# Kernel tuning notes

Hardware: AMD Instinct MI355X
Metric: run time of the kernel (lower is better)

Reference implementation:

```python
import jax, jax.numpy as jnp
import numpy as np

H = 8  # num_heads

def setup_inputs() -> dict:
    key = jax.random.key(0)
    ks = jax.random.split(key, 10)
    B, N, C = 2048, 50, 256
    x = jax.random.normal(ks[0], (B, N, C), dtype=jnp.float32)
    adj = jax.random.uniform(ks[1], (B, N, N), dtype=jnp.float32)
    matrix = jax.random.normal(ks[2], (B, N, N), dtype=jnp.float32)
    s = 0.02
    Wq = jax.random.normal(ks[3], (C, C), dtype=jnp.float32) * s
    bq = jnp.zeros((C,), dtype=jnp.float32)
    Wk = jax.random.normal(ks[4], (C, C), dtype=jnp.float32) * s
    bk = jnp.zeros((C,), dtype=jnp.float32)
    Wa = jax.random.normal(ks[5], (N * H, N), dtype=jnp.float32) * s
    ba = jnp.zeros((N * H,), dtype=jnp.float32)
    Wm = jax.random.normal(ks[6], (N * H, N), dtype=jnp.float32) * s
    bm = jnp.zeros((N * H,), dtype=jnp.float32)
    lambdas = jnp.tile(jnp.array([[1.0, 0.0, 0.0]], dtype=jnp.float32), (H, 1))
    return {"x": x, "adj": adj, "matrix": matrix, "Wq": Wq, "bq": bq,
            "Wk": Wk, "bk": bk, "Wa": Wa, "ba": ba, "Wm": Wm, "bm": bm,
            "lambdas": lambdas}

def reference(x, adj, matrix, Wq, bq, Wk, bk, Wa, ba, Wm, bm, lambdas):
    B, N, C = x.shape
    D = C // H
    # torch Linear: y = x @ W.T + b
    q = (jnp.einsum('bnc,dc->bnd', x, Wq) + bq).reshape(B, N, H, D).transpose(0, 2, 1, 3)
    k = (jnp.einsum('bnc,dc->bnd', x, Wk) + bk).reshape(B, N, H, D).transpose(0, 2, 1, 3)
    # NOTE: original code computes v with self.k (faithful to source)
    v = k
    # scale uses full dim C (x.shape[-1]), not head_dim, as in source
    attn = jax.nn.softmax(jnp.einsum('bhnd,bhmd->bhnm', q, k) * (C ** -0.5), axis=-1)
    adj_a = jax.nn.softmax(
        (jnp.einsum('bnm,km->bnk', adj, Wa) + ba).reshape(B, N, H, N).transpose(0, 2, 1, 3), axis=-1)
    mat_a = jax.nn.softmax(
        (jnp.einsum('bnm,km->bnk', matrix, Wm) + bm).reshape(B, N, H, N).transpose(0, 2, 1, 3), axis=-1)
    lam = jax.nn.softmax(lambdas, axis=-1)  # [H, 3]
    l0 = lam[:, 0][None, :, None, None]
    l1 = lam[:, 1][None, :, None, None]
    l2 = lam[:, 2][None, :, None, None]
    mix = l0 * attn + l1 * adj_a + l2 * mat_a  # [B, H, N, N]
    out = jnp.einsum('bhnm,bhmd->bhnd', mix, v).transpose(0, 2, 1, 3).reshape(B, N, C)
    return out
```

## Files before the change

kernel.cpp:

```cpp
#include <hip/hip_runtime.h>
#include <stdint.h>


typedef __attribute__((ext_vector_type(8))) short short8;
typedef __attribute__((ext_vector_type(4))) float f32x4;
typedef unsigned short u16;

__device__ __forceinline__ u16 f2bf(float f) {
  unsigned int u = __float_as_uint(f);
  u = (u + 0x7FFFu + ((u >> 16) & 1u)) >> 16;
  return (u16)u;
}
__device__ __forceinline__ unsigned cvt_pk_bf16(float a, float b) {
  unsigned r;
  asm("v_cvt_pk_bf16_f32 %0, %1, %2" : "=v"(r) : "v"(a), "v"(b));
  return r;
}

__global__ __launch_bounds__(256) void castW(const float* __restrict__ Wq,
                                             const float* __restrict__ Wk,
                                             u16* __restrict__ dst) {
  int idx8 = blockIdx.x * 256 + threadIdx.x;
  int r = idx8 >> 5, c = (idx8 & 31) * 8;
  const float* src = (r < 256) ? (Wq + (size_t)r * 256 + c)
                               : (Wk + (size_t)(r - 256) * 256 + c);
  float4 v0 = *(const float4*)(src);
  float4 v1 = *(const float4*)(src + 4);
  short8 o;
  o[0] = f2bf(v0.x); o[1] = f2bf(v0.y); o[2] = f2bf(v0.z); o[3] = f2bf(v0.w);
  o[4] = f2bf(v1.x); o[5] = f2bf(v1.y); o[6] = f2bf(v1.z); o[7] = f2bf(v1.w);
  *(short8*)(dst + (size_t)idx8 * 8) = o;
}

__global__ __launch_bounds__(256) void castS(const float* __restrict__ Wa,
                                             const float* __restrict__ Wm,
                                             u16* __restrict__ da, u16* __restrict__ dm) {
  int idx = blockIdx.x * 256 + threadIdx.x;
  int r = idx >> 6, c = idx & 63;
  float va = 0.f, vm = 0.f;
  if (r < 400 && c < 50) { va = Wa[r * 50 + c]; vm = Wm[r * 50 + c]; }
  da[idx] = f2bf(va); dm[idx] = f2bf(vm);
}

__global__ __launch_bounds__(256) void castA(const float* __restrict__ adj,
                                             const float* __restrict__ mat,
                                             u16* __restrict__ da, u16* __restrict__ dm) {
  const int total8 = (102416 * 64) / 8;
  int stride = gridDim.x * 256;
  for (int i8 = blockIdx.x * 256 + threadIdx.x; i8 < total8; i8 += stride) {
    int r = i8 >> 3, c = (i8 & 7) * 8;
    short8 oa = (short8){0,0,0,0,0,0,0,0};
    short8 om = (short8){0,0,0,0,0,0,0,0};
    if (r < 102400) {
      size_t base = (size_t)r * 50;
#pragma unroll
      for (int p = 0; p < 4; ++p) {
        int col = c + 2 * p;
        if (col < 50) {
          float2 va = *(const float2*)(adj + base + col);
          float2 vm = *(const float2*)(mat + base + col);
          oa[2*p] = f2bf(va.x); oa[2*p+1] = f2bf(va.y);
          om[2*p] = f2bf(vm.x); om[2*p+1] = f2bf(vm.y);
        }
      }
    }
    *(short8*)(da + (size_t)i8 * 8) = oa;
    *(short8*)(dm + (size_t)i8 * 8) = om;
  }
}

__global__ __launch_bounds__(256) void proj_kernel(
    const float* __restrict__ x, const u16* __restrict__ wqk,
    const float* __restrict__ bq, const float* __restrict__ bk,
    u16* __restrict__ qws, u16* __restrict__ kws) {
  __shared__ char xa[64 * 512];
  __shared__ char wb[64 * 512];
  const int tid = threadIdx.x;
  const int m0 = blockIdx.x * 64;

#pragma unroll
  for (int t = 0; t < 16; ++t) {
    int idx = tid + t * 256;
    int r = idx >> 6, c4 = idx & 63;
    float4 v = *(const float4*)(x + (size_t)(m0 + r) * 256 + c4 * 4);
    unsigned long long pk = (unsigned long long)f2bf(v.x)
                          | ((unsigned long long)f2bf(v.y) << 16)
                          | ((unsigned long long)f2bf(v.z) << 32)
                          | ((unsigned long long)f2bf(v.w) << 48);
    int byte = (r * 512 + c4 * 8) ^ ((r & 7) << 4);
    *(unsigned long long*)(xa + byte) = pk;
  }
  __syncthreads();

  const int w = tid >> 6, l = tid & 63, lo = l & 15, g = l >> 4;
  short8 a[8];
  const int ra = 16 * w + lo;
#pragma unroll
  for (int ks = 0; ks < 8; ++ks)
    a[ks] = *(const short8*)(xa + ((ra * 512 + ks * 64 + g * 16) ^ ((ra & 7) << 4)));
  size_t mb[4];
#pragma unroll
  for (int i = 0; i < 4; ++i) {
    int m = m0 + 16 * w + 4 * g + i;
    int b = m / 50;
    int n = m - 50 * b;
    mb[i] = (size_t)b * 12800 + (size_t)n * 32;
  }

  for (int nt = 0; nt < 8; ++nt) {
    __syncthreads();
#pragma unroll
    for (int t = 0; t < 8; ++t) {
      int idx = tid + t * 256;
      int r = idx >> 5, c8 = idx & 31;
      short8 v = *(const short8*)(wqk + (size_t)(nt * 64 + r) * 256 + c8 * 8);
      int byte = (r * 512 + c8 * 16) ^ ((r & 7) << 4);
      *(short8*)(wb + byte) = v;
    }
    __syncthreads();

    f32x4 acc[4];
#pragma unroll
    for (int tj = 0; tj < 4; ++tj) acc[tj] = (f32x4){0.f, 0.f, 0.f, 0.f};
#pragma unroll
    for (int ks = 0; ks < 8; ++ks) {
#pragma unroll
      for (int tj = 0; tj < 4; ++tj) {
        int rb = 16 * tj + lo;
        short8 bb = *(const short8*)(wb + ((rb * 512 + ks * 64 + g * 16) ^ ((rb & 7) << 4)));
        acc[tj] = __builtin_amdgcn_mfma_f32_16x16x32_bf16(a[ks], bb, acc[tj], 0, 0, 0);
      }
    }
    const int n0 = nt * 64;
#pragma unroll
    for (int tj = 0; tj < 4; ++tj) {
      int j = n0 + 16 * tj + lo;
      int jj = j & 255;
      float bias = (j < 256) ? bq[jj] : bk[jj];
      u16* dst = (j < 256) ? qws : kws;
      int hh = jj >> 5, d = jj & 31;
#pragma unroll
      for (int i = 0; i < 4; ++i)
        dst[mb[i] + (size_t)hh * 1600 + d] = f2bf(acc[tj][i] + bias);
    }
  }
}


__device__ __forceinline__ void lds_fence() {
  asm volatile("s_waitcnt lgkmcnt(0)" ::: "memory");
  __builtin_amdgcn_sched_barrier(0);
}

__device__ __forceinline__ void softmax_store(f32x4 (&S)[4], const float (&bias)[4][4],
                                              float scale, float lam,
                                              u16* sh, int tj, int lo, int g) {
  float mx = -3.0e38f;
#pragma unroll
  for (int ti = 0; ti < 4; ++ti)
#pragma unroll
    for (int i = 0; i < 4; ++i) {
      float v = S[ti][i] * scale + bias[ti][i];
      S[ti][i] = v;
      mx = fmaxf(mx, v);
    }
  mx = fmaxf(mx, __shfl_xor(mx, 16));
  mx = fmaxf(mx, __shfl_xor(mx, 32));
  float sum = 0.f;
#pragma unroll
  for (int ti = 0; ti < 4; ++ti)
#pragma unroll
    for (int i = 0; i < 4; ++i) {
      float p = __expf(S[ti][i] - mx);
      S[ti][i] = p;
      sum += p;
    }
  sum += __shfl_xor(sum, 16);
  sum += __shfl_xor(sum, 32);
  float r = lam * __builtin_amdgcn_rcpf(sum);
  const int n = lo + 16 * tj;
#pragma unroll
  for (int ti = 0; ti < 4; ++ti) {
    uint2 pk;
    pk.x = cvt_pk_bf16(S[ti][0] * r, S[ti][1] * r);
    pk.y = cvt_pk_bf16(S[ti][2] * r, S[ti][3] * r);
    *(uint2*)(sh + n * 72 + 16 * ti + 4 * g) = pk;
  }
}

__device__ __forceinline__ void pv_accum(const u16* sh, const short8 (&vb)[2][2],
                                         f32x4 (&O)[4][2], int lo, int g) {
  lds_fence();
#pragma unroll
  for (int ks = 0; ks < 2; ++ks) {
    short8 pa[4];
#pragma unroll
    for (int ti = 0; ti < 4; ++ti)
      pa[ti] = *(const short8*)(sh + (lo + 16 * ti) * 72 + ks * 32 + g * 8);
#pragma unroll
    for (int tjv = 0; tjv < 2; ++tjv)
#pragma unroll
      for (int ti = 0; ti < 4; ++ti)
        O[ti][tjv] = __builtin_amdgcn_mfma_f32_16x16x32_bf16(pa[ti], vb[tjv][ks], O[ti][tjv], 0, 0, 0);
  }
}

__device__ __forceinline__ void adj_phase(const u16* __restrict__ aBase,
                                          const u16* __restrict__ bBase,
                                          const float* __restrict__ biasPtr,
                                          float lam, u16* sh, const short8 (&vb)[2][2],
                                          f32x4 (&O)[4][2], int lo, int g) {
  short8 af[4][2];
#pragma unroll
  for (int ti = 0; ti < 4; ++ti)
#pragma unroll
    for (int ks = 0; ks < 2; ++ks)
      af[ti][ks] = *(const short8*)(aBase + (size_t)(lo + 16 * ti) * 64 + ks * 32 + g * 8);
  float bias[4][4];
#pragma unroll
  for (int ti = 0; ti < 4; ++ti)
#pragma unroll
    for (int i = 0; i < 4; ++i) {
      int m = 16 * ti + 4 * g + i;
      bias[ti][i] = (m < 50) ? biasPtr[m] : -1.0e30f;
    }
#pragma unroll
  for (int tj = 0; tj < 4; ++tj) {
    f32x4 S[4];
#pragma unroll
    for (int ti = 0; ti < 4; ++ti) S[ti] = (f32x4){0.f, 0.f, 0.f, 0.f};
#pragma unroll
    for (int ks = 0; ks < 2; ++ks) {
      short8 bf8 = *(const short8*)(bBase + (size_t)(lo + 16 * tj) * 64 + ks * 32 + g * 8);
#pragma unroll
      for (int ti = 0; ti < 4; ++ti)
        S[ti] = __builtin_amdgcn_mfma_f32_16x16x32_bf16(af[ti][ks], bf8, S[ti], 0, 0, 0);
    }
    softmax_store(S, bias, 1.0f, lam, sh, tj, lo, g);
  }
  pv_accum(sh, vb, O, lo, g);
}

__global__ __launch_bounds__(256) void attn_kernel(
    const u16* __restrict__ qws, const u16* __restrict__ kws,
    const u16* __restrict__ adjb, const u16* __restrict__ matb,
    const u16* __restrict__ wab, const u16* __restrict__ wmb,
    const float* __restrict__ ba, const float* __restrict__ bm,
    const float* __restrict__ lambdas, float* __restrict__ out) {
  __shared__ u16 smem[4][4608];
  const int tid = threadIdx.x;
  const int w = tid >> 6, l = tid & 63, lo = l & 15, g = l >> 4;
  const int bh = blockIdx.x * 4 + w;
  const int b = bh >> 3, h = bh & 7;
  u16* sh = smem[w];

  float la = lambdas[h * 3 + 0], lb = lambdas[h * 3 + 1], lc = lambdas[h * 3 + 2];
  float lmx = fmaxf(la, fmaxf(lb, lc));
  float e0 = __expf(la - lmx), e1 = __expf(lb - lmx), e2 = __expf(lc - lmx);
  float einv = 1.f / (e0 + e1 + e2);
  float lam0 = e0 * einv, lam1 = e1 * einv, lam2 = e2 * einv;

  {
    const u16* kr = kws + ((size_t)bh * 50 + l) * 32;
#pragma unroll
    for (int ch = 0; ch < 4; ++ch) {
      short8 v = (short8){0, 0, 0, 0, 0, 0, 0, 0};
      if (l < 50) v = *(const short8*)(kr + ch * 8);
#pragma unroll
      for (int jj = 0; jj < 8; ++jj)
        sh[(ch * 8 + jj) * 72 + l] = (u16)v[jj];
    }
  }
  lds_fence();
  short8 vb[2][2];
#pragma unroll
  for (int tjv = 0; tjv < 2; ++tjv)
#pragma unroll
    for (int ks = 0; ks < 2; ++ks)
      vb[tjv][ks] = *(const short8*)(sh + (lo + 16 * tjv) * 72 + ks * 32 + g * 8);

  f32x4 O[4][2];
#pragma unroll
  for (int ti = 0; ti < 4; ++ti)
#pragma unroll
    for (int tjv = 0; tjv < 2; ++tjv) O[ti][tjv] = (f32x4){0.f, 0.f, 0.f, 0.f};

  {
    short8 af[4];
#pragma unroll
    for (int ti = 0; ti < 4; ++ti)
      af[ti] = *(const short8*)(kws + ((size_t)bh * 50 + lo + 16 * ti) * 32 + g * 8);
    float bias[4][4];
#pragma unroll
    for (int ti = 0; ti < 4; ++ti)
#pragma unroll
      for (int i = 0; i < 4; ++i)
        bias[ti][i] = (16 * ti + 4 * g + i < 50) ? 0.f : -1.0e30f;
#pragma unroll
    for (int tj = 0; tj < 4; ++tj) {
      short8 qf = *(const short8*)(qws + ((size_t)bh * 50 + lo + 16 * tj) * 32 + g * 8);
      f32x4 S[4];
#pragma unroll
      for (int ti = 0; ti < 4; ++ti) S[ti] = (f32x4){0.f, 0.f, 0.f, 0.f};
#pragma unroll
      for (int ti = 0; ti < 4; ++ti)
        S[ti] = __builtin_amdgcn_mfma_f32_16x16x32_bf16(af[ti], qf, S[ti], 0, 0, 0);
      softmax_store(S, bias, 0.0625f, lam0, sh, tj, lo, g);
    }
    pv_accum(sh, vb, O, lo, g);
  }
  adj_phase(wab + (size_t)h * 50 * 64, adjb + (size_t)b * 50 * 64, ba + h * 50,
            lam1, sh, vb, O, lo, g);
  adj_phase(wmb + (size_t)h * 50 * 64, matb + (size_t)b * 50 * 64, bm + h * 50,
            lam2, sh, vb, O, lo, g);

  float* ob = out + ((size_t)b * 50) * 256 + h * 32;
#pragma unroll
  for (int ti = 0; ti < 4; ++ti)
#pragma unroll
    for (int i = 0; i < 4; ++i) {
      int n = 16 * ti + 4 * g + i;
      if (n < 50) {
#pragma unroll
        for (int tjv = 0; tjv < 2; ++tjv)
          ob[(size_t)n * 256 + 16 * tjv + lo] = O[ti][tjv][i];
      }
    }
}

extern "C" void kernel_launch(void* const* d_in, const int* in_sizes, int n_in,
                              void* d_out, int out_size, void* d_ws, size_t ws_size,
                              hipStream_t stream) {
  const float* x       = (const float*)d_in[0];
  const float* adj     = (const float*)d_in[1];
  const float* mat     = (const float*)d_in[2];
  const float* Wq      = (const float*)d_in[3];
  const float* bq      = (const float*)d_in[4];
  const float* Wk      = (const float*)d_in[5];
  const float* bk      = (const float*)d_in[6];
  const float* Wa      = (const float*)d_in[7];
  const float* ba      = (const float*)d_in[8];
  const float* Wm      = (const float*)d_in[9];
  const float* bm      = (const float*)d_in[10];
  const float* lambdas = (const float*)d_in[11];
  float* out = (float*)d_out;

  char* ws = (char*)d_ws;
  u16* wqk  = (u16*)ws; ws += (size_t)512 * 256 * 2;
  u16* wab  = (u16*)ws; ws += (size_t)416 * 64 * 2;
  u16* wmb  = (u16*)ws; ws += (size_t)416 * 64 * 2;
  u16* adjb = (u16*)ws; ws += (size_t)102416 * 64 * 2;
  u16* matb = (u16*)ws; ws += (size_t)102416 * 64 * 2;
  u16* qws  = (u16*)ws; ws += (size_t)819264 * 32 * 2;
  u16* kws  = (u16*)ws; ws += (size_t)819264 * 32 * 2;

  castW<<<64, 256, 0, stream>>>(Wq, Wk, wqk);
  castS<<<104, 256, 0, stream>>>(Wa, Wm, wab, wmb);
  castA<<<2048, 256, 0, stream>>>(adj, mat, adjb, matb);
  proj_kernel<<<1600, 256, 0, stream>>>(x, wqk, bq, bk, qws, kws);
  attn_kernel<<<4096, 256, 0, stream>>>(qws, kws, adjb, matb, wab, wmb, ba, bm, lambdas, out);
}
```

Before: 218.9 us.

## Merge cast kernels and fuse per-tile softmax with PV accumulation

Folds the three cast launches into one kernel that also zeroes the padding rows of the q/k workspace. The attention softmax is restructured to process one query tile at a time and immediately feed it into the PV MFMAs through a double-buffered LDS slot. This halves shared memory per block and shortens register live ranges. The max-subtraction is dropped and exp2 is used with log2e folded into scale and bias. Skipping the max is only safe while logits stay small, which adds overflow risk for larger inputs.

```diff
diff --git a/kernel.cpp b/kernel.cpp
--- a/kernel.cpp
+++ b/kernel.cpp
@@ -5,6 +5,8 @@
 typedef __attribute__((ext_vector_type(8))) short short8;
 typedef __attribute__((ext_vector_type(4))) float f32x4;
 typedef unsigned short u16;
+
+#define L2E 1.4426950408889634f
 
 __device__ __forceinline__ u16 f2bf(float f) {
   unsigned int u = __float_as_uint(f);
@@ -16,56 +18,68 @@
   asm("v_cvt_pk_bf16_f32 %0, %1, %2" : "=v"(r) : "v"(a), "v"(b));
   return r;
 }
-
-__global__ __launch_bounds__(256) void castW(const float* __restrict__ Wq,
-                                             const float* __restrict__ Wk,
-                                             u16* __restrict__ dst) {
-  int idx8 = blockIdx.x * 256 + threadIdx.x;
-  int r = idx8 >> 5, c = (idx8 & 31) * 8;
-  const float* src = (r < 256) ? (Wq + (size_t)r * 256 + c)
-                               : (Wk + (size_t)(r - 256) * 256 + c);
-  float4 v0 = *(const float4*)(src);
-  float4 v1 = *(const float4*)(src + 4);
-  short8 o;
-  o[0] = f2bf(v0.x); o[1] = f2bf(v0.y); o[2] = f2bf(v0.z); o[3] = f2bf(v0.w);
-  o[4] = f2bf(v1.x); o[5] = f2bf(v1.y); o[6] = f2bf(v1.z); o[7] = f2bf(v1.w);
-  *(short8*)(dst + (size_t)idx8 * 8) = o;
-}
-
-__global__ __launch_bounds__(256) void castS(const float* __restrict__ Wa,
-                                             const float* __restrict__ Wm,
-                                             u16* __restrict__ da, u16* __restrict__ dm) {
-  int idx = blockIdx.x * 256 + threadIdx.x;
-  int r = idx >> 6, c = idx & 63;
-  float va = 0.f, vm = 0.f;
-  if (r < 400 && c < 50) { va = Wa[r * 50 + c]; vm = Wm[r * 50 + c]; }
-  da[idx] = f2bf(va); dm[idx] = f2bf(vm);
-}
-
-__global__ __launch_bounds__(256) void castA(const float* __restrict__ adj,
-                                             const float* __restrict__ mat,
-                                             u16* __restrict__ da, u16* __restrict__ dm) {
-  const int total8 = (102416 * 64) / 8;
-  int stride = gridDim.x * 256;
-  for (int i8 = blockIdx.x * 256 + threadIdx.x; i8 < total8; i8 += stride) {
-    int r = i8 >> 3, c = (i8 & 7) * 8;
-    short8 oa = (short8){0,0,0,0,0,0,0,0};
-    short8 om = (short8){0,0,0,0,0,0,0,0};
-    if (r < 102400) {
-      size_t base = (size_t)r * 50;
-#pragma unroll
-      for (int p = 0; p < 4; ++p) {
-        int col = c + 2 * p;
-        if (col < 50) {
-          float2 va = *(const float2*)(adj + base + col);
-          float2 vm = *(const float2*)(mat + base + col);
-          oa[2*p] = f2bf(va.x); oa[2*p+1] = f2bf(va.y);
-          om[2*p] = f2bf(vm.x); om[2*p+1] = f2bf(vm.y);
+__device__ __forceinline__ float exp2_fast(float x) {
+#if __has_builtin(__builtin_amdgcn_exp2f)
+  return __builtin_amdgcn_exp2f(x);
+#else
+  return __expf(x * 0.6931471805599453f);
+#endif
+}
+__device__ __forceinline__ void lds_fence() {
+  asm volatile("s_waitcnt lgkmcnt(0)" ::: "memory");
+}
+
+__global__ __launch_bounds__(256) void cast_all(
+    const float* __restrict__ adj, const float* __restrict__ mat,
+    const float* __restrict__ Wq, const float* __restrict__ Wk,
+    const float* __restrict__ Wa, const float* __restrict__ Wm,
+    u16* __restrict__ da, u16* __restrict__ dm, u16* __restrict__ wqk,
+    u16* __restrict__ wab, u16* __restrict__ wmb,
+    u16* __restrict__ qws, u16* __restrict__ kws) {
+  const int blk = blockIdx.x, tid = threadIdx.x;
+  if (blk < 2048) {
+    const int total8 = (102416 * 64) / 8;
+    for (int i8 = blk * 256 + tid; i8 < total8; i8 += 2048 * 256) {
+      int r = i8 >> 3, c = (i8 & 7) * 8;
+      short8 oa = (short8){0,0,0,0,0,0,0,0};
+      short8 om = (short8){0,0,0,0,0,0,0,0};
+      if (r < 102400) {
+        size_t base = (size_t)r * 50;
+#pragma unroll
+        for (int p = 0; p < 4; ++p) {
+          int col = c + 2 * p;
+          if (col < 50) {
+            float2 va = *(const float2*)(adj + base + col);
+            float2 vm = *(const float2*)(mat + base + col);
+            oa[2*p] = f2bf(va.x); oa[2*p+1] = f2bf(va.y);
+            om[2*p] = f2bf(vm.x); om[2*p+1] = f2bf(vm.y);
+          }
         }
       }
-    }
-    *(short8*)(da + (size_t)i8 * 8) = oa;
-    *(short8*)(dm + (size_t)i8 * 8) = om;
+      *(short8*)(da + (size_t)i8 * 8) = oa;
+      *(short8*)(dm + (size_t)i8 * 8) = om;
+    }
+  } else if (blk < 2112) {
+    int idx8 = (blk - 2048) * 256 + tid;
+    int r = idx8 >> 5, c = (idx8 & 31) * 8;
+    const float* src = (r < 256) ? (Wq + (size_t)r * 256 + c)
+                                 : (Wk + (size_t)(r - 256) * 256 + c);
+    float4 v0 = *(const float4*)(src);
+    float4 v1 = *(const float4*)(src + 4);
+    short8 o;
+    o[0] = f2bf(v0.x); o[1] = f2bf(v0.y); o[2] = f2bf(v0.z); o[3] = f2bf(v0.w);
+    o[4] = f2bf(v1.x); o[5] = f2bf(v1.y); o[6] = f2bf(v1.z); o[7] = f2bf(v1.w);
+    *(short8*)(wqk + (size_t)idx8 * 8) = o;
+  } else if (blk < 2216) {
+    int idx = (blk - 2112) * 256 + tid;
+    int r = idx >> 6, c = idx & 63;
+    float va = 0.f, vm = 0.f;
+    if (r < 400 && c < 50) { va = Wa[r * 50 + c]; vm = Wm[r * 50 + c]; }
+    wab[idx] = f2bf(va); wmb[idx] = f2bf(vm);
+  } else {
+    short8 z = (short8){0,0,0,0,0,0,0,0};
+    *(short8*)(qws + (size_t)819200 * 32 + tid * 8) = z;
+    *(short8*)(kws + (size_t)819200 * 32 + tid * 8) = z;
   }
 }
 
@@ -146,99 +160,74 @@
   }
 }
 
-
-__device__ __forceinline__ void lds_fence() {
-  asm volatile("s_waitcnt lgkmcnt(0)" ::: "memory");
-  __builtin_amdgcn_sched_barrier(0);
-}
-
-__device__ __forceinline__ void softmax_store(f32x4 (&S)[4], const float (&bias)[4][4],
-                                              float scale, float lam,
-                                              u16* sh, int tj, int lo, int g) {
-  float mx = -3.0e38f;
-#pragma unroll
-  for (int ti = 0; ti < 4; ++ti)
-#pragma unroll
-    for (int i = 0; i < 4; ++i) {
-      float v = S[ti][i] * scale + bias[ti][i];
-      S[ti][i] = v;
-      mx = fmaxf(mx, v);
-    }
-  mx = fmaxf(mx, __shfl_xor(mx, 16));
-  mx = fmaxf(mx, __shfl_xor(mx, 32));
-  float sum = 0.f;
-#pragma unroll
-  for (int ti = 0; ti < 4; ++ti)
-#pragma unroll
-    for (int i = 0; i < 4; ++i) {
-      float p = __expf(S[ti][i] - mx);
-      S[ti][i] = p;
-      sum += p;
-    }
+__device__ __forceinline__ void sm_pv_tile(
+    f32x4 (&S)[4], const float (&bml)[4][4], float sl2e, float lam,
+    u16* pb, const short8 (&vb)[2][2], f32x4 (&Otj)[2], int tj, int lo, int g) {
+  float p[4][4];
+#pragma unroll
+  for (int ti = 0; ti < 4; ++ti)
+#pragma unroll
+    for (int i = 0; i < 4; ++i)
+      p[ti][i] = exp2_fast(S[ti][i] * sl2e + bml[ti][i]);
+  float t0 = (p[0][0] + p[0][1]) + (p[0][2] + p[0][3]);
+  float t1 = (p[1][0] + p[1][1]) + (p[1][2] + p[1][3]);
+  float t2 = (p[2][0] + p[2][1]) + (p[2][2] + p[2][3]);
+  float t3 = (p[3][0] + p[3][1]) + (p[3][2] + p[3][3]);
+  float sum = (t0 + t1) + (t2 + t3);
   sum += __shfl_xor(sum, 16);
   sum += __shfl_xor(sum, 32);
   float r = lam * __builtin_amdgcn_rcpf(sum);
-  const int n = lo + 16 * tj;
+  u16* base = pb + (tj & 1) * 1152 + lo * 72;
 #pragma unroll
   for (int ti = 0; ti < 4; ++ti) {
     uint2 pk;
-    pk.x = cvt_pk_bf16(S[ti][0] * r, S[ti][1] * r);
-    pk.y = cvt_pk_bf16(S[ti][2] * r, S[ti][3] * r);
-    *(uint2*)(sh + n * 72 + 16 * ti + 4 * g) = pk;
-  }
-}
-
-__device__ __forceinline__ void pv_accum(const u16* sh, const short8 (&vb)[2][2],
-                                         f32x4 (&O)[4][2], int lo, int g) {
+    pk.x = cvt_pk_bf16(p[ti][0] * r, p[ti][1] * r);
+    pk.y = cvt_pk_bf16(p[ti][2] * r, p[ti][3] * r);
+    *(uint2*)(base + 16 * ti + 4 * g) = pk;
+  }
   lds_fence();
 #pragma unroll
   for (int ks = 0; ks < 2; ++ks) {
-    short8 pa[4];
-#pragma unroll
-    for (int ti = 0; ti < 4; ++ti)
-      pa[ti] = *(const short8*)(sh + (lo + 16 * ti) * 72 + ks * 32 + g * 8);
+    short8 pa = *(const short8*)(pb + (tj & 1) * 1152 + lo * 72 + ks * 32 + g * 8);
 #pragma unroll
     for (int tjv = 0; tjv < 2; ++tjv)
-#pragma unroll
-      for (int ti = 0; ti < 4; ++ti)
-        O[ti][tjv] = __builtin_amdgcn_mfma_f32_16x16x32_bf16(pa[ti], vb[tjv][ks], O[ti][tjv], 0, 0, 0);
-  }
-}
-
-__device__ __forceinline__ void adj_phase(const u16* __restrict__ aBase,
-                                          const u16* __restrict__ bBase,
-                                          const float* __restrict__ biasPtr,
-                                          float lam, u16* sh, const short8 (&vb)[2][2],
-                                          f32x4 (&O)[4][2], int lo, int g) {
+      Otj[tjv] = __builtin_amdgcn_mfma_f32_16x16x32_bf16(pa, vb[tjv][ks], Otj[tjv], 0, 0, 0);
+  }
+}
+
+__device__ __forceinline__ void adj_phase(
+    const u16* __restrict__ aBase, const u16* __restrict__ bBase,
+    const float* __restrict__ biasPtr, float lam,
+    u16* pb, const short8 (&vb)[2][2], f32x4 (&O)[4][2], int lo, int g) {
   short8 af[4][2];
 #pragma unroll
   for (int ti = 0; ti < 4; ++ti)
 #pragma unroll
     for (int ks = 0; ks < 2; ++ks)
       af[ti][ks] = *(const short8*)(aBase + (size_t)(lo + 16 * ti) * 64 + ks * 32 + g * 8);
-  float bias[4][4];
+  float bml[4][4];
 #pragma unroll
   for (int ti = 0; ti < 4; ++ti)
 #pragma unroll
     for (int i = 0; i < 4; ++i) {
       int m = 16 * ti + 4 * g + i;
-      bias[ti][i] = (m < 50) ? biasPtr[m] : -1.0e30f;
+      bml[ti][i] = (m < 50) ? biasPtr[m] * L2E : -1.0e30f;
     }
 #pragma unroll
   for (int tj = 0; tj < 4; ++tj) {
+    short8 bf0 = *(const short8*)(bBase + (size_t)(lo + 16 * tj) * 64 + g * 8);
+    short8 bf1 = *(const short8*)(bBase + (size_t)(lo + 16 * tj) * 64 + 32 + g * 8);
     f32x4 S[4];
 #pragma unroll
     for (int ti = 0; ti < 4; ++ti) S[ti] = (f32x4){0.f, 0.f, 0.f, 0.f};
 #pragma unroll
-    for (int ks = 0; ks < 2; ++ks) {
-      short8 bf8 = *(const short8*)(bBase + (size_t)(lo + 16 * tj) * 64 + ks * 32 + g * 8);
-#pragma unroll
-      for (int ti = 0; ti < 4; ++ti)
-        S[ti] = __builtin_amdgcn_mfma_f32_16x16x32_bf16(af[ti][ks], bf8, S[ti], 0, 0, 0);
-    }
-    softmax_store(S, bias, 1.0f, lam, sh, tj, lo, g);
-  }
-  pv_accum(sh, vb, O, lo, g);
+    for (int ti = 0; ti < 4; ++ti)
+      S[ti] = __builtin_amdgcn_mfma_f32_16x16x32_bf16(af[ti][0], bf0, S[ti], 0, 0, 0);
+#pragma unroll
+    for (int ti = 0; ti < 4; ++ti)
+      S[ti] = __builtin_amdgcn_mfma_f32_16x16x32_bf16(af[ti][1], bf1, S[ti], 0, 0, 0);
+    sm_pv_tile(S, bml, L2E, lam, pb, vb, O[tj], tj, lo, g);
+  }
 }
 
 __global__ __launch_bounds__(256) void attn_kernel(
@@ -247,7 +236,7 @@
     const u16* __restrict__ wab, const u16* __restrict__ wmb,
     const float* __restrict__ ba, const float* __restrict__ bm,
     const float* __restrict__ lambdas, float* __restrict__ out) {
-  __shared__ u16 smem[4][4608];
+  __shared__ u16 smem[4][2304];
   const int tid = threadIdx.x;
   const int w = tid >> 6, l = tid & 63, lo = l & 15, g = l >> 4;
   const int bh = blockIdx.x * 4 + w;
@@ -261,7 +250,7 @@
   float lam0 = e0 * einv, lam1 = e1 * einv, lam2 = e2 * einv;
 
   {
-    const u16* kr = kws + ((size_t)bh * 50 + l) * 32;
+    const u16* kr = kws + (size_t)bh * 1600 + (size_t)l * 32;
 #pragma unroll
     for (int ch = 0; ch < 4; ++ch) {
       short8 v = (short8){0, 0, 0, 0, 0, 0, 0, 0};
@@ -289,29 +278,28 @@
     short8 af[4];
 #pragma unroll
     for (int ti = 0; ti < 4; ++ti)
-      af[ti] = *(const short8*)(kws + ((size_t)bh * 50 + lo + 16 * ti) * 32 + g * 8);
-    float bias[4][4];
+      af[ti] = *(const short8*)(kws + (size_t)bh * 1600 + (size_t)(lo + 16 * ti) * 32 + g * 8);
+    float bml[4][4];
 #pragma unroll
     for (int ti = 0; ti < 4; ++ti)
 #pragma unroll
       for (int i = 0; i < 4; ++i)
-        bias[ti][i] = (16 * ti + 4 * g + i < 50) ? 0.f : -1.0e30f;
+        bml[ti][i] = (16 * ti + 4 * g + i < 50) ? 0.f : -1.0e30f;
 #pragma unroll
     for (int tj = 0; tj < 4; ++tj) {
-      short8 qf = *(const short8*)(qws + ((size_t)bh * 50 + lo + 16 * tj) * 32 + g * 8);
+      short8 qf = *(const short8*)(qws + (size_t)bh * 1600 + (size_t)(lo + 16 * tj) * 32 + g * 8);
       f32x4 S[4];
 #pragma unroll
       for (int ti = 0; ti < 4; ++ti) S[ti] = (f32x4){0.f, 0.f, 0.f, 0.f};
 #pragma unroll
       for (int ti = 0; ti < 4; ++ti)
         S[ti] = __builtin_amdgcn_mfma_f32_16x16x32_bf16(af[ti], qf, S[ti], 0, 0, 0);
-      softmax_store(S, bias, 0.0625f, lam0, sh, tj, lo, g);
-    }
-    pv_accum(sh, vb, O, lo, g);
-  }
-  adj_phase(wab + (size_t)h * 50 * 64, adjb + (size_t)b * 50 * 64, ba + h * 50,
+      sm_pv_tile(S, bml, 0.0625f * L2E, lam0, sh, vb, O[tj], tj, lo, g);
+    }
+  }
+  adj_phase(wab + (size_t)h * 3200, adjb + (size_t)b * 3200, ba + h * 50,
             lam1, sh, vb, O, lo, g);
-  adj_phase(wmb + (size_t)h * 50 * 64, matb + (size_t)b * 50 * 64, bm + h * 50,
+  adj_phase(wmb + (size_t)h * 3200, matb + (size_t)b * 3200, bm + h * 50,
             lam2, sh, vb, O, lo, g);
 
   float* ob = out + ((size_t)b * 50) * 256 + h * 32;
@@ -354,9 +342,8 @@
   u16* qws  = (u16*)ws; ws += (size_t)819264 * 32 * 2;
   u16* kws  = (u16*)ws; ws += (size_t)819264 * 32 * 2;
 
-  castW<<<64, 256, 0, stream>>>(Wq, Wk, wqk);
-  castS<<<104, 256, 0, stream>>>(Wa, Wm, wab, wmb);
-  castA<<<2048, 256, 0, stream>>>(adj, mat, adjb, matb);
+  cast_all<<<2217, 256, 0, stream>>>(adj, mat, Wq, Wk, Wa, Wm,
+                                     adjb, matb, wqk, wab, wmb, qws, kws);
   proj_kernel<<<1600, 256, 0, stream>>>(x, wqk, bq, bk, qws, kws);
   attn_kernel<<<4096, 256, 0, stream>>>(qws, kws, adjb, matb, wab, wmb, ba, bm, lambdas, out);
 }
```

After: 203.9 us. 1.07x faster.
